# Kernel tuning notes

Hardware: AMD Instinct MI355X
Metric: run time of the kernel (lower is better)

The kernel has to match this reference:

```python
import jax, jax.numpy as jnp
from jax import lax
import numpy as np

B, CIN, CP, H, W = 16, 64, 64, 64, 64
K1 = 3   # deformable kernel
K2 = 5   # parallel conv kernel
EPS = 1e-5


def conv2d(x, w, stride, pad):
    return lax.conv_general_dilated(
        x, w, (stride, stride), [(pad, pad), (pad, pad)],
        dimension_numbers=('NCHW', 'OIHW', 'NCHW'))


def batchnorm(x, g, b, m, v):
    scale = g / jnp.sqrt(v + EPS)
    return (x - m[None, :, None, None]) * scale[None, :, None, None] + b[None, :, None, None]


def deform_conv2d(x, offset, weight, stride, pad):
    # x: [B,Cin,H,W], offset: [B,2*K*K,Ho,Wo] (dy,dx interleaved per kernel tap, torchvision layout)
    Bn, Cin, Hn, Wn = x.shape
    Cout, _, K, _ = weight.shape
    KK = K * K
    Ho, Wo = offset.shape[2], offset.shape[3]
    off = offset.reshape(Bn, KK, 2, Ho, Wo)
    dy, dx = off[:, :, 0], off[:, :, 1]                      # [B,KK,Ho,Wo]
    ky, kx = jnp.meshgrid(jnp.arange(K), jnp.arange(K), indexing='ij')
    ky = ky.reshape(KK).astype(x.dtype)
    kx = kx.reshape(KK).astype(x.dtype)
    base_y = (jnp.arange(Ho) * stride - pad).astype(x.dtype)
    base_x = (jnp.arange(Wo) * stride - pad).astype(x.dtype)
    ys = base_y[None, None, :, None] + ky[None, :, None, None] + dy  # [B,KK,Ho,Wo]
    xs = base_x[None, None, None, :] + kx[None, :, None, None] + dx
    y0 = jnp.floor(ys); x0 = jnp.floor(xs)
    wy1 = ys - y0; wx1 = xs - x0
    wy0 = 1.0 - wy1; wx0 = 1.0 - wx1
    flat = x.reshape(Bn, Cin, Hn * Wn)

    def gather(yi, xi):
        valid = ((yi >= 0) & (yi <= Hn - 1) & (xi >= 0) & (xi <= Wn - 1))
        yc = jnp.clip(yi, 0, Hn - 1).astype(jnp.int32)
        xc = jnp.clip(xi, 0, Wn - 1).astype(jnp.int32)
        idx = (yc * Wn + xc).reshape(Bn, -1)                 # [B,KK*Ho*Wo]
        g = jax.vmap(lambda f, i: jnp.take(f, i, axis=1))(flat, idx)
        g = g.reshape(Bn, Cin, KK, Ho, Wo)
        return g * valid.astype(x.dtype)[:, None]

    val = (gather(y0, x0) * (wy0 * wx0)[:, None]
           + gather(y0, x0 + 1) * (wy0 * wx1)[:, None]
           + gather(y0 + 1, x0) * (wy1 * wx0)[:, None]
           + gather(y0 + 1, x0 + 1) * (wy1 * wx1)[:, None])   # [B,Cin,KK,Ho,Wo]
    w_r = weight.reshape(Cout, Cin, KK)
    return jnp.einsum('bcknm,ock->bonm', val, w_r)


def setup_inputs():
    key = jax.random.key(0)
    ks = jax.random.split(key, 18)
    f32 = jnp.float32
    x = jax.random.normal(ks[0], (B, CIN, H, W), f32)
    w_off = jax.random.normal(ks[1], (2 * K1 * K1, CIN, 3, 3), f32) * 0.01
    b_off = jnp.zeros((2 * K1 * K1,), f32)
    w1 = jax.random.normal(ks[2], (CP, CIN, K1, K1), f32) / np.sqrt(CIN * K1 * K1)
    w3 = jax.random.normal(ks[3], (CP, CIN, K2, K2), f32) / np.sqrt(CIN * K2 * K2)
    w2 = jax.random.normal(ks[4], (CP, CP, 3, 3), f32) / np.sqrt(CP * 9)
    def bn(i):
        g = jax.random.uniform(ks[5 + 4 * i], (CP,), f32, 0.5, 1.5)
        b = jax.random.normal(ks[6 + 4 * i], (CP,), f32) * 0.1
        m = jax.random.normal(ks[7 + 4 * i], (CP,), f32) * 0.1
        v = jax.random.uniform(ks[8 + 4 * i], (CP,), f32, 0.5, 1.5)
        return g, b, m, v
    g1, b1, m1, v1 = bn(0)
    g3, b3, m3, v3 = bn(1)
    g2, b2, m2, v2 = bn(2)
    return dict(x=x, w_off=w_off, b_off=b_off, w1=w1, g1=g1, b1=b1, m1=m1, v1=v1,
                w3=w3, g3=g3, b3=b3, m3=m3, v3=v3, w2=w2, g2=g2, b2=b2, m2=m2, v2=v2)


def reference(x, w_off, b_off, w1, g1, b1, m1, v1, w3, g3, b3, m3, v3, w2, g2, b2, m2, v2):
    offset1 = conv2d(x, w_off, 1, 1) + b_off[None, :, None, None]
    out = jax.nn.relu(batchnorm(deform_conv2d(x, offset1, w1, 1, 1), g1, b1, m1, v1))
    out_1 = jax.nn.relu(batchnorm(conv2d(x, w3, 1, 2), g3, b3, m3, v3))
    out = out + out_1
    out = batchnorm(conv2d(out, w2, 1, 1), g2, b2, m2, v2)
    out = out + x  # identity shortcut (stride=1, in_planes==planes)
    return jax.nn.relu(out)
```

## Files before the change

### kernel.cpp

```cpp
#include <hip/hip_runtime.h>
#include <hip/hip_bf16.h>


#define EPSv 1e-5f
#define XP 68

typedef __attribute__((ext_vector_type(8))) short bf16x8;
typedef __attribute__((ext_vector_type(16))) float f32x16;
typedef __attribute__((ext_vector_type(2))) float f32x2;

__device__ inline ushort f2bf(float f) {
  __hip_bfloat16 h = __float2bfloat16(f);
  return *(ushort*)&h;
}
__device__ inline float bitsf(unsigned int u) {
  union { unsigned int i; float f; } c; c.i = u; return c.f;
}

__global__ __launch_bounds__(256) void prep_kernel(
    const float* __restrict__ x, const float* __restrict__ w3,
    const float* __restrict__ w2, const float* __restrict__ w1,
    const float* __restrict__ w_off,
    ushort* __restrict__ xTp, ushort* __restrict__ w3F,
    ushort* __restrict__ w2F, ushort* __restrict__ w1F,
    ushort* __restrict__ wofF) {
  __shared__ float tile[64][65];
  const int blk = blockIdx.x;
  if (blk < 1024) {
    const int y = blk & 63, b = blk >> 6;
    for (int i = threadIdx.x; i < 4096; i += 256) {
      int ci = i >> 6, xx = i & 63;
      tile[ci][xx] = x[(((size_t)b * 64 + ci) * 64 + y) * 64 + xx];
    }
    __syncthreads();
    for (int i = threadIdx.x; i < 2048; i += 256) {
      int xx = i >> 5, cip = (i & 31) * 2;
      ushort2 v;
      v.x = f2bf(tile[cip][xx]);
      v.y = f2bf(tile[cip + 1][xx]);
      *(ushort2*)&xTp[(((size_t)(b * 64 + y) * XP) + (xx + 2)) * 64 + cip] = v;
    }
    if (threadIdx.x < 128) {
      int colid = threadIdx.x >> 5;
      int col = (colid & 1) + (colid >> 1) * 66;
      int cip = (threadIdx.x & 31) * 2;
      ushort2 z; z.x = 0; z.y = 0;
      *(ushort2*)&xTp[(((size_t)(b * 64 + y) * XP) + col) * 64 + cip] = z;
    }
    return;
  }
  int idx = (blk - 1024) * 256 + threadIdx.x;
  if (idx < 102400) {
    int j = idx & 7, lane = (idx >> 3) & 63, ks = (idx >> 9) & 3;
    int half = (idx >> 11) & 1, kk = idx >> 12;
    int ln = lane & 31, kh = lane >> 5;
    int co = half * 32 + ln, ci = ks * 16 + kh * 8 + j;
    w3F[idx] = f2bf(w3[(co * 64 + ci) * 25 + kk]);
    return;
  }
  idx -= 102400;
  if (idx < 36864) {
    int j = idx & 7, lane = (idx >> 3) & 63, ks = (idx >> 9) & 3;
    int half = (idx >> 11) & 1, kk = idx >> 12;
    int ln = lane & 31, kh = lane >> 5;
    int co = half * 32 + ln, ci = ks * 16 + kh * 8 + j;
    w2F[idx] = f2bf(w2[(co * 64 + ci) * 9 + kk]);
    return;
  }
  idx -= 36864;
  if (idx < 36864) {
    int j = idx & 7, lane = (idx >> 3) & 63, ks = (idx >> 9) & 3;
    int half = (idx >> 11) & 1, kk = idx >> 12;
    int ln = lane & 31, kh = lane >> 5;
    int co = half * 32 + ln, ci = ks * 16 + kh * 8 + j;
    w1F[idx] = f2bf(w1[(co * 64 + ci) * 9 + kk]);
    return;
  }
  idx -= 36864;
  if (idx < 18432) {
    int j = idx & 7, lane = (idx >> 3) & 63, ks = (idx >> 9) & 3;
    int kk = idx >> 11;
    int ln = lane & 31, kh = lane >> 5;
    int ci = ks * 16 + kh * 8 + j;
    wofF[idx] = f2bf(ln < 18 ? w_off[(ln * 64 + ci) * 9 + kk] : 0.f);
  }
}

__device__ __forceinline__ bf16x8 blend4(bf16x8 va, bf16x8 vb, bf16x8 vc, bf16x8 vd,
                                         f32x2 w00v, f32x2 w01v, f32x2 w10v, f32x2 w11v) {
  const unsigned int* ua = (const unsigned int*)&va;
  const unsigned int* ub = (const unsigned int*)&vb;
  const unsigned int* uc = (const unsigned int*)&vc;
  const unsigned int* ud = (const unsigned int*)&vd;
  bf16x8 f;
  ushort2* fo = (ushort2*)&f;
#pragma unroll
  for (int d = 0; d < 4; ++d) {
    f32x2 av = {bitsf(ua[d] << 16), bitsf(ua[d] & 0xFFFF0000u)};
    f32x2 bv = {bitsf(ub[d] << 16), bitsf(ub[d] & 0xFFFF0000u)};
    f32x2 cv = {bitsf(uc[d] << 16), bitsf(uc[d] & 0xFFFF0000u)};
    f32x2 dv = {bitsf(ud[d] << 16), bitsf(ud[d] & 0xFFFF0000u)};
    f32x2 r = w00v * av + w01v * bv + w10v * cv + w11v * dv;
    __hip_bfloat162 h2 = __float22bfloat162_rn(make_float2(r.x, r.y));
    fo[d] = *(ushort2*)&h2;
  }
  return f;
}

__global__ __launch_bounds__(256, 2) void fused_kernel(
    const ushort* __restrict__ xTp, const ushort* __restrict__ wofF,
    const float* __restrict__ b_off, const ushort* __restrict__ w1F,
    const ushort* __restrict__ w3F,
    const float* __restrict__ g1, const float* __restrict__ b1,
    const float* __restrict__ m1, const float* __restrict__ v1,
    const float* __restrict__ g3, const float* __restrict__ b3,
    const float* __restrict__ m3, const float* __restrict__ v3,
    ushort* __restrict__ s1T) {
  __shared__ __align__(16) uint4 ldsx[6 * 68 * 8];
  __shared__ float stash[2 * 64 * 18];
  __shared__ float bn1s[64], bn1b[64], bn3s[64], bn3b[64];

  const int tid = threadIdx.x;
  const int wv = tid >> 6, lane = tid & 63;
  const int ln = lane & 31, kh = lane >> 5;
  const int r = wv >> 1, nt = wv & 1;
  const int y0 = blockIdx.x * 2, b = blockIdx.y;
  const int y = y0 + r, px = nt * 32 + ln;
  const uint4* xT4 = (const uint4*)xTp;
  const ushort* xb = xTp + (size_t)b * 64 * XP * 64;
  const bool interior = (y0 >= 2 && y0 <= 60);

  if (tid < 64) {
    float s = g1[tid] * rsqrtf(v1[tid] + EPSv);
    bn1s[tid] = s; bn1b[tid] = b1[tid] - m1[tid] * s;
    float s3 = g3[tid] * rsqrtf(v3[tid] + EPSv);
    bn3s[tid] = s3; bn3b[tid] = b3[tid] - m3[tid] * s3;
  }
  for (int i = tid; i < 6 * 68 * 8; i += 256) {
    int tr = i / (68 * 8), rem = i % (68 * 8);
    int col = rem >> 3, c = rem & 7;
    int ysrc = min(max(y0 - 2 + tr, 0), 63);
    uint4 v = xT4[((size_t)((b * 64 + ysrc) * XP + col)) * 8 + c];
    ldsx[(tr * 68 + col) * 8 + (c ^ (col & 7))] = v;
  }
  __syncthreads();

  f32x16 acco;
#pragma unroll
  for (int j = 0; j < 16; ++j) acco[j] = 0.f;
  if (interior) {
#pragma unroll
    for (int kk = 0; kk < 9; ++kk) {
      const int ky = kk / 3, kx = kk % 3;
      const int tr = r + ky + 1;
      const int col = px + kx + 1;
      bf16x8 af[4], bf[4];
#pragma unroll
      for (int ks = 0; ks < 4; ++ks)
        af[ks] = *(const bf16x8*)&wofF[(size_t)((kk * 4 + ks) * 64 + lane) * 8];
#pragma unroll
      for (int ks = 0; ks < 4; ++ks) {
        int c = ks * 2 + kh;
        bf[ks] = *(const bf16x8*)&ldsx[(tr * 68 + col) * 8 + (c ^ (col & 7))];
      }
#pragma unroll
      for (int ks = 0; ks < 4; ++ks)
        acco = __builtin_amdgcn_mfma_f32_32x32x16_bf16(af[ks], bf[ks], acco, 0, 0, 0);
    }
  } else {
#pragma unroll
    for (int kk = 0; kk < 9; ++kk) {
      const int ky = kk / 3, kx = kk % 3;
      const int yy = y - 1 + ky;
      if (yy >= 0 && yy <= 63) {
        const int tr = yy - (y0 - 2);
        const int col = px + kx + 1;
#pragma unroll
        for (int ks = 0; ks < 4; ++ks) {
          int c = ks * 2 + kh;
          bf16x8 af = *(const bf16x8*)&wofF[(size_t)((kk * 4 + ks) * 64 + lane) * 8];
          bf16x8 bf = *(const bf16x8*)&ldsx[(tr * 68 + col) * 8 + (c ^ (col & 7))];
          acco = __builtin_amdgcn_mfma_f32_32x32x16_bf16(af, bf, acco, 0, 0, 0);
        }
      }
    }
  }
#pragma unroll
  for (int reg = 0; reg < 16; ++reg) {
    int co = (reg & 3) + 8 * (reg >> 2) + 4 * kh;
    if (co < 18)
      stash[(r * 64 + px) * 18 + co] = acco[reg] + b_off[co];
  }
  asm volatile("" ::: "memory");

  float dyv[9], dxv[9];
#pragma unroll
  for (int kk = 0; kk < 9; ++kk) {
    dyv[kk] = stash[(r * 64 + px) * 18 + 2 * kk];
    dxv[kk] = stash[(r * 64 + px) * 18 + 2 * kk + 1];
  }
  bool fast = true;
#pragma unroll
  for (int kk = 0; kk < 9; ++kk) {
    int iy0 = (int)floorf((float)(y - 1 + kk / 3) + dyv[kk]);
    int iy1 = iy0 + 1;
    bool ok0 = (iy0 < 0) || (iy0 > 63) || (iy0 >= y0 - 2 && iy0 <= y0 + 3);
    bool ok1 = (iy1 < 0) || (iy1 > 63) || (iy1 >= y0 - 2 && iy1 <= y0 + 3);
    fast = fast && ok0 && ok1;
  }

  f32x16 accd0, accd1;
#pragma unroll
  for (int j = 0; j < 16; ++j) { accd0[j] = 0.f; accd1[j] = 0.f; }

  if (__ballot(!fast) == 0ull) {
#pragma unroll
    for (int kk = 0; kk < 9; ++kk) {
      const int ky = kk / 3, kx = kk % 3;
      float ys = (float)(y - 1 + ky) + dyv[kk];
      float xs = (float)(px - 1 + kx) + dxv[kk];
      float y0f = floorf(ys), x0f = floorf(xs);
      float wy1 = ys - y0f, wx1 = xs - x0f;
      float wy0 = 1.f - wy1, wx0 = 1.f - wx1;
      int iy0 = (int)y0f, ix0 = (int)x0f;
      int iy1 = iy0 + 1, ix1 = ix0 + 1;
      float vy0 = (iy0 >= 0 && iy0 <= 63) ? 1.f : 0.f;
      float vy1 = (iy1 >= 0 && iy1 <= 63) ? 1.f : 0.f;
      float vx0 = (ix0 >= 0 && ix0 <= 63) ? 1.f : 0.f;
      float vx1 = (ix1 >= 0 && ix1 <= 63) ? 1.f : 0.f;
      int x0c = min(max(ix0, 0), 63), x1c = min(max(ix1, 0), 63);
      float w00 = wy0 * wx0 * vy0 * vx0;
      float w01 = wy0 * wx1 * vy0 * vx1;
      float w10 = wy1 * wx0 * vy1 * vx0;
      float w11 = wy1 * wx1 * vy1 * vx1;
      int tr0 = min(max(iy0 - (y0 - 2), 0), 5);
      int tr1 = min(max(iy1 - (y0 - 2), 0), 5);
      int c0 = x0c + 2, c1 = x1c + 2;
      f32x2 w00v = {w00, w00}, w01v = {w01, w01};
      f32x2 w10v = {w10, w10}, w11v = {w11, w11};

      bf16x8 a0[4], a1[4], va[4], vb[4], vc[4], vd[4];
#pragma unroll
      for (int ks = 0; ks < 4; ++ks) {
        a0[ks] = *(const bf16x8*)&w1F[(size_t)(((kk * 2 + 0) * 4 + ks) * 64 + lane) * 8];
        a1[ks] = *(const bf16x8*)&w1F[(size_t)(((kk * 2 + 1) * 4 + ks) * 64 + lane) * 8];
      }
#pragma unroll
      for (int ks = 0; ks < 4; ++ks) {
        int c = ks * 2 + kh;
        va[ks] = *(const bf16x8*)&ldsx[(tr0 * 68 + c0) * 8 + (c ^ (c0 & 7))];
        vb[ks] = *(const bf16x8*)&ldsx[(tr0 * 68 + c1) * 8 + (c ^ (c1 & 7))];
        vc[ks] = *(const bf16x8*)&ldsx[(tr1 * 68 + c0) * 8 + (c ^ (c0 & 7))];
        vd[ks] = *(const bf16x8*)&ldsx[(tr1 * 68 + c1) * 8 + (c ^ (c1 & 7))];
      }
#pragma unroll
      for (int ks = 0; ks < 4; ++ks) {
        bf16x8 f = blend4(va[ks], vb[ks], vc[ks], vd[ks], w00v, w01v, w10v, w11v);
        accd0 = __builtin_amdgcn_mfma_f32_32x32x16_bf16(a0[ks], f, accd0, 0, 0, 0);
        accd1 = __builtin_amdgcn_mfma_f32_32x32x16_bf16(a1[ks], f, accd1, 0, 0, 0);
      }
    }
  } else {
#pragma unroll
    for (int kk = 0; kk < 9; ++kk) {
      const int ky = kk / 3, kx = kk % 3;
      float ys = (float)(y - 1 + ky) + dyv[kk];
      float xs = (float)(px - 1 + kx) + dxv[kk];
      float y0f = floorf(ys), x0f = floorf(xs);
      float wy1 = ys - y0f, wx1 = xs - x0f;
      float wy0 = 1.f - wy1, wx0 = 1.f - wx1;
      int iy0 = (int)y0f, ix0 = (int)x0f;
      int iy1 = iy0 + 1, ix1 = ix0 + 1;
      float vy0 = (iy0 >= 0 && iy0 <= 63) ? 1.f : 0.f;
      float vy1 = (iy1 >= 0 && iy1 <= 63) ? 1.f : 0.f;
      float vx0 = (ix0 >= 0 && ix0 <= 63) ? 1.f : 0.f;
      float vx1 = (ix1 >= 0 && ix1 <= 63) ? 1.f : 0.f;
      int x0c = min(max(ix0, 0), 63), x1c = min(max(ix1, 0), 63);
      int y0c = min(max(iy0, 0), 63), y1c = min(max(iy1, 0), 63);
      float w00 = wy0 * wx0 * vy0 * vx0;
      float w01 = wy0 * wx1 * vy0 * vx1;
      float w10 = wy1 * wx0 * vy1 * vx0;
      float w11 = wy1 * wx1 * vy1 * vx1;
      int tr0 = min(max(iy0 - (y0 - 2), 0), 5);
      int tr1 = min(max(iy1 - (y0 - 2), 0), 5);
      int c0 = x0c + 2, c1 = x1c + 2;
      f32x2 w00v = {w00, w00}, w01v = {w01, w01};
      f32x2 w10v = {w10, w10}, w11v = {w11, w11};

      bf16x8 frag[4];
#pragma unroll
      for (int ks = 0; ks < 4; ++ks) {
        int c = ks * 2 + kh;
        bf16x8 va = *(const bf16x8*)&ldsx[(tr0 * 68 + c0) * 8 + (c ^ (c0 & 7))];
        bf16x8 vb = *(const bf16x8*)&ldsx[(tr0 * 68 + c1) * 8 + (c ^ (c1 & 7))];
        bf16x8 vc = *(const bf16x8*)&ldsx[(tr1 * 68 + c0) * 8 + (c ^ (c0 & 7))];
        bf16x8 vd = *(const bf16x8*)&ldsx[(tr1 * 68 + c1) * 8 + (c ^ (c1 & 7))];
        frag[ks] = blend4(va, vb, vc, vd, w00v, w01v, w10v, w11v);
      }
      if (!fast) {
        const ushort* p00 = xb + ((size_t)(y0c * XP + x0c + 2)) * 64 + kh * 8;
        const ushort* p01 = xb + ((size_t)(y0c * XP + x1c + 2)) * 64 + kh * 8;
        const ushort* p10 = xb + ((size_t)(y1c * XP + x0c + 2)) * 64 + kh * 8;
        const ushort* p11 = xb + ((size_t)(y1c * XP + x1c + 2)) * 64 + kh * 8;
#pragma unroll
        for (int ks = 0; ks < 4; ++ks) {
          bf16x8 va = *(const bf16x8*)(p00 + ks * 16);
          bf16x8 vb = *(const bf16x8*)(p01 + ks * 16);
          bf16x8 vc = *(const bf16x8*)(p10 + ks * 16);
          bf16x8 vd = *(const bf16x8*)(p11 + ks * 16);
          frag[ks] = blend4(va, vb, vc, vd, w00v, w01v, w10v, w11v);
        }
      }
#pragma unroll
      for (int ks = 0; ks < 4; ++ks) {
        bf16x8 a0 = *(const bf16x8*)&w1F[(size_t)(((kk * 2 + 0) * 4 + ks) * 64 + lane) * 8];
        bf16x8 a1 = *(const bf16x8*)&w1F[(size_t)(((kk * 2 + 1) * 4 + ks) * 64 + lane) * 8];
        accd0 = __builtin_amdgcn_mfma_f32_32x32x16_bf16(a0, frag[ks], accd0, 0, 0, 0);
        accd1 = __builtin_amdgcn_mfma_f32_32x32x16_bf16(a1, frag[ks], accd1, 0, 0, 0);
      }
    }
  }

  f32x16 acc50, acc51;
#pragma unroll
  for (int j = 0; j < 16; ++j) { acc50[j] = 0.f; acc51[j] = 0.f; }
  if (interior) {
#pragma unroll
    for (int kk = 0; kk < 25; ++kk) {
      const int ky = kk / 5, kx = kk % 5;
      const int tr = r + ky;
      const int col = px + kx;
      bf16x8 a0[4], a1[4], bfv[4];
#pragma unroll
      for (int ks = 0; ks < 4; ++ks) {
        a0[ks] = *(const bf16x8*)&w3F[(size_t)(((kk * 2 + 0) * 4 + ks) * 64 + lane) * 8];
        a1[ks] = *(const bf16x8*)&w3F[(size_t)(((kk * 2 + 1) * 4 + ks) * 64 + lane) * 8];
      }
#pragma unroll
      for (int ks = 0; ks < 4; ++ks) {
        int c = ks * 2 + kh;
        bfv[ks] = *(const bf16x8*)&ldsx[(tr * 68 + col) * 8 + (c ^ (col & 7))];
      }
#pragma unroll
      for (int ks = 0; ks < 4; ++ks) {
        acc50 = __builtin_amdgcn_mfma_f32_32x32x16_bf16(a0[ks], bfv[ks], acc50, 0, 0, 0);
        acc51 = __builtin_amdgcn_mfma_f32_32x32x16_bf16(a1[ks], bfv[ks], acc51, 0, 0, 0);
      }
    }
  } else {
#pragma unroll
    for (int kk = 0; kk < 25; ++kk) {
      const int ky = kk / 5, kx = kk % 5;
      const int yy = y - 2 + ky;
      if (yy >= 0 && yy <= 63) {
        const int tr = r + ky;
        const int col = px + kx;
#pragma unroll
        for (int ks = 0; ks < 4; ++ks) {
          int c = ks * 2 + kh;
          bf16x8 bf = *(const bf16x8*)&ldsx[(tr * 68 + col) * 8 + (c ^ (col & 7))];
          bf16x8 a0 = *(const bf16x8*)&w3F[(size_t)(((kk * 2 + 0) * 4 + ks) * 64 + lane) * 8];
          bf16x8 a1 = *(const bf16x8*)&w3F[(size_t)(((kk * 2 + 1) * 4 + ks) * 64 + lane) * 8];
          acc50 = __builtin_amdgcn_mfma_f32_32x32x16_bf16(a0, bf, acc50, 0, 0, 0);
          acc51 = __builtin_amdgcn_mfma_f32_32x32x16_bf16(a1, bf, acc51, 0, 0, 0);
        }
      }
    }
  }

  ushort* op = s1T + ((size_t)((b * 64 + y) * 64 + px)) * 64;
#pragma unroll
  for (int q = 0; q < 4; ++q) {
    int co0 = 8 * q + 4 * kh;
    float vv[4];
#pragma unroll
    for (int rr = 0; rr < 4; ++rr) {
      int co = co0 + rr;
      float vd = accd0[q * 4 + rr] * bn1s[co] + bn1b[co];
      vd = vd > 0.f ? vd : 0.f;
      float v5 = acc50[q * 4 + rr] * bn3s[co] + bn3b[co];
      v5 = v5 > 0.f ? v5 : 0.f;
      vv[rr] = vd + v5;
    }
    ushort4 st;
    st.x = f2bf(vv[0]); st.y = f2bf(vv[1]); st.z = f2bf(vv[2]); st.w = f2bf(vv[3]);
    *(ushort4*)(op + co0) = st;
#pragma unroll
    for (int rr = 0; rr < 4; ++rr) {
      int co = co0 + 32 + rr;
      float vd = accd1[q * 4 + rr] * bn1s[co] + bn1b[co];
      vd = vd > 0.f ? vd : 0.f;
      float v5 = acc51[q * 4 + rr] * bn3s[co] + bn3b[co];
      v5 = v5 > 0.f ? v5 : 0.f;
      vv[rr] = vd + v5;
    }
    st.x = f2bf(vv[0]); st.y = f2bf(vv[1]); st.z = f2bf(vv[2]); st.w = f2bf(vv[3]);
    *(ushort4*)(op + co0 + 32) = st;
  }
}

__global__ __launch_bounds__(256, 2) void conv3_mfma_kernel(
    const ushort* __restrict__ s1T, const ushort* __restrict__ w2F,
    const float* __restrict__ g2, const float* __restrict__ b2,
    const float* __restrict__ m2, const float* __restrict__ v2,
    const float* __restrict__ x, float* __restrict__ out) {
  __shared__ __align__(16) uint4 Bt[3 * 66 * 8];
  __shared__ float sc[64], bi[64];
  const int tid = threadIdx.x;
  if (tid < 64) {
    float s = g2[tid] * rsqrtf(v2[tid] + EPSv);
    sc[tid] = s;
    bi[tid] = b2[tid] - m2[tid] * s;
  }
  const int y = blockIdx.x, b = blockIdx.y;
  const int wv = tid >> 6, lane = tid & 63;
  const int ln = lane & 31, kh = lane >> 5;
  const int mh = wv & 1, nt = wv >> 1;
  const int px = nt * 32 + ln;
  const uint4* s1T4 = (const uint4*)s1T;

  for (int i = tid; i < 3 * 66 * 8; i += 256) {
    int tr = i / (66 * 8), rem = i % (66 * 8);
    int col = rem >> 3, c = rem & 7;
    int yy = y - 1 + tr, xcol = col - 1;
    uint4 v = make_uint4(0, 0, 0, 0);
    if (yy >= 0 && yy <= 63 && xcol >= 0 && xcol <= 63)
      v = s1T4[((size_t)((b * 64 + yy) * 64 + xcol)) * 8 + c];
    Bt[(tr * 66 + col) * 8 + (c ^ (col & 7))] = v;
  }
  __syncthreads();

  f32x16 acc;
#pragma unroll
  for (int j = 0; j < 16; ++j) acc[j] = 0.f;

#pragma unroll
  for (int kk = 0; kk < 9; ++kk) {
    const int ky = kk / 3, kx = kk % 3;
    const int col = px + kx;
    bf16x8 af[4], bfr[4];
#pragma unroll
    for (int ccb = 0; ccb < 4; ++ccb)
      af[ccb] = *(const bf16x8*)&w2F[(size_t)(((kk * 2 + mh) * 4 + ccb) * 64 + lane) * 8];
#pragma unroll
    for (int ccb = 0; ccb < 4; ++ccb) {
      int c = ccb * 2 + kh;
      bfr[ccb] = *(const bf16x8*)&Bt[(ky * 66 + col) * 8 + (c ^ (col & 7))];
    }
#pragma unroll
    for (int ccb = 0; ccb < 4; ++ccb)
      acc = __builtin_amdgcn_mfma_f32_32x32x16_bf16(af[ccb], bfr[ccb], acc, 0, 0, 0);
  }
#pragma unroll
  for (int reg = 0; reg < 16; ++reg) {
    int co = (reg & 3) + 8 * (reg >> 2) + 4 * kh + mh * 32;
    size_t o = (((size_t)b * 64 + co) * 64 + y) * 64 + px;
    float v = acc[reg] * sc[co] + bi[co] + x[o];
    out[o] = v > 0.f ? v : 0.f;
  }
}

extern "C" void kernel_launch(void* const* d_in, const int* in_sizes, int n_in,
                              void* d_out, int out_size, void* d_ws, size_t ws_size,
                              hipStream_t stream) {
  const float* x     = (const float*)d_in[0];
  const float* w_off = (const float*)d_in[1];
  const float* b_off = (const float*)d_in[2];
  const float* w1    = (const float*)d_in[3];
  const float* g1    = (const float*)d_in[4];
  const float* b1    = (const float*)d_in[5];
  const float* m1    = (const float*)d_in[6];
  const float* v1    = (const float*)d_in[7];
  const float* w3    = (const float*)d_in[8];
  const float* g3    = (const float*)d_in[9];
  const float* b3    = (const float*)d_in[10];
  const float* m3    = (const float*)d_in[11];
  const float* v3    = (const float*)d_in[12];
  const float* w2    = (const float*)d_in[13];
  const float* g2    = (const float*)d_in[14];
  const float* b2    = (const float*)d_in[15];
  const float* m2    = (const float*)d_in[16];
  const float* v2    = (const float*)d_in[17];
  float* out = (float*)d_out;

  ushort* xTp  = (ushort*)d_ws;
  ushort* s1T  = xTp + (size_t)16 * 64 * XP * 64;
  ushort* w3F  = s1T + (size_t)16 * 64 * 64 * 64;
  ushort* w2F  = w3F + 102400;
  ushort* w1F  = w2F + 36864;
  ushort* wofF = w1F + 36864;

  prep_kernel<<<dim3(1024 + 760), dim3(256), 0, stream>>>(x, w3, w2, w1, w_off,
                                                          xTp, w3F, w2F, w1F, wofF);
  fused_kernel<<<dim3(32, 16), dim3(256), 0, stream>>>(xTp, wofF, b_off, w1F, w3F,
                                                       g1, b1, m1, v1, g3, b3, m3, v3,
                                                       s1T);
  conv3_mfma_kernel<<<dim3(64, 16), dim3(256), 0, stream>>>(s1T, w2F, g2, b2, m2, v2,
                                                            x, out);
}
```

Before: 68.02 us.

## Interleave deformable and 5x5 conv MFMA loops; pass offsets via lane shuffles

The offset values produced by the offset conv are now exchanged between the two half-waves with __shfl_xor instead of being staged through an LDS stash array, which removes that shared buffer and its round trip. For interior blocks where all samples fall in the LDS tile, the deformable 3x3 taps and the 5x5 conv taps are interleaved in one loop, so the bilinear blend VALU work can overlap with independent MFMA chains. This keeps four accumulators live at once, which raises register pressure and could hurt occupancy or cause spills.

```diff
diff --git a/kernel.cpp b/kernel.cpp
--- a/kernel.cpp
+++ b/kernel.cpp
@@ -117,7 +117,6 @@
     const float* __restrict__ m3, const float* __restrict__ v3,
     ushort* __restrict__ s1T) {
   __shared__ __align__(16) uint4 ldsx[6 * 68 * 8];
-  __shared__ float stash[2 * 64 * 18];
   __shared__ float bn1s[64], bn1b[64], bn3s[64], bn3b[64];
 
   const int tid = threadIdx.x;
@@ -185,19 +184,20 @@
       }
     }
   }
-#pragma unroll
-  for (int reg = 0; reg < 16; ++reg) {
-    int co = (reg & 3) + 8 * (reg >> 2) + 4 * kh;
-    if (co < 18)
-      stash[(r * 64 + px) * 18 + co] = acco[reg] + b_off[co];
-  }
-  asm volatile("" ::: "memory");
-
+  float oth[10];
+#pragma unroll
+  for (int t = 0; t < 10; ++t) oth[t] = __shfl_xor(acco[t], 32);
   float dyv[9], dxv[9];
 #pragma unroll
   for (int kk = 0; kk < 9; ++kk) {
-    dyv[kk] = stash[(r * 64 + px) * 18 + 2 * kk];
-    dxv[kk] = stash[(r * 64 + px) * 18 + 2 * kk + 1];
+    const int cY = 2 * kk, cX = 2 * kk + 1;
+    const int rY = (cY & 3) + 4 * (cY >> 3);
+    const int rX = (cX & 3) + 4 * (cX >> 3);
+    const int sY = (cY >> 2) & 1, sX = (cX >> 2) & 1;
+    float vy = (sY == kh) ? acco[rY] : oth[rY];
+    float vx = (sX == kh) ? acco[rX] : oth[rX];
+    dyv[kk] = vy + b_off[cY];
+    dxv[kk] = vx + b_off[cX];
   }
   bool fast = true;
 #pragma unroll
@@ -208,161 +208,230 @@
     bool ok1 = (iy1 < 0) || (iy1 > 63) || (iy1 >= y0 - 2 && iy1 <= y0 + 3);
     fast = fast && ok0 && ok1;
   }
-
-  f32x16 accd0, accd1;
-#pragma unroll
-  for (int j = 0; j < 16; ++j) { accd0[j] = 0.f; accd1[j] = 0.f; }
-
-  if (__ballot(!fast) == 0ull) {
-#pragma unroll
-    for (int kk = 0; kk < 9; ++kk) {
-      const int ky = kk / 3, kx = kk % 3;
-      float ys = (float)(y - 1 + ky) + dyv[kk];
-      float xs = (float)(px - 1 + kx) + dxv[kk];
-      float y0f = floorf(ys), x0f = floorf(xs);
-      float wy1 = ys - y0f, wx1 = xs - x0f;
-      float wy0 = 1.f - wy1, wx0 = 1.f - wx1;
-      int iy0 = (int)y0f, ix0 = (int)x0f;
-      int iy1 = iy0 + 1, ix1 = ix0 + 1;
-      float vy0 = (iy0 >= 0 && iy0 <= 63) ? 1.f : 0.f;
-      float vy1 = (iy1 >= 0 && iy1 <= 63) ? 1.f : 0.f;
-      float vx0 = (ix0 >= 0 && ix0 <= 63) ? 1.f : 0.f;
-      float vx1 = (ix1 >= 0 && ix1 <= 63) ? 1.f : 0.f;
-      int x0c = min(max(ix0, 0), 63), x1c = min(max(ix1, 0), 63);
-      float w00 = wy0 * wx0 * vy0 * vx0;
-      float w01 = wy0 * wx1 * vy0 * vx1;
-      float w10 = wy1 * wx0 * vy1 * vx0;
-      float w11 = wy1 * wx1 * vy1 * vx1;
-      int tr0 = min(max(iy0 - (y0 - 2), 0), 5);
-      int tr1 = min(max(iy1 - (y0 - 2), 0), 5);
-      int c0 = x0c + 2, c1 = x1c + 2;
-      f32x2 w00v = {w00, w00}, w01v = {w01, w01};
-      f32x2 w10v = {w10, w10}, w11v = {w11, w11};
-
-      bf16x8 a0[4], a1[4], va[4], vb[4], vc[4], vd[4];
-#pragma unroll
-      for (int ks = 0; ks < 4; ++ks) {
-        a0[ks] = *(const bf16x8*)&w1F[(size_t)(((kk * 2 + 0) * 4 + ks) * 64 + lane) * 8];
-        a1[ks] = *(const bf16x8*)&w1F[(size_t)(((kk * 2 + 1) * 4 + ks) * 64 + lane) * 8];
-      }
-#pragma unroll
-      for (int ks = 0; ks < 4; ++ks) {
-        int c = ks * 2 + kh;
-        va[ks] = *(const bf16x8*)&ldsx[(tr0 * 68 + c0) * 8 + (c ^ (c0 & 7))];
-        vb[ks] = *(const bf16x8*)&ldsx[(tr0 * 68 + c1) * 8 + (c ^ (c1 & 7))];
-        vc[ks] = *(const bf16x8*)&ldsx[(tr1 * 68 + c0) * 8 + (c ^ (c0 & 7))];
-        vd[ks] = *(const bf16x8*)&ldsx[(tr1 * 68 + c1) * 8 + (c ^ (c1 & 7))];
-      }
-#pragma unroll
-      for (int ks = 0; ks < 4; ++ks) {
-        bf16x8 f = blend4(va[ks], vb[ks], vc[ks], vd[ks], w00v, w01v, w10v, w11v);
-        accd0 = __builtin_amdgcn_mfma_f32_32x32x16_bf16(a0[ks], f, accd0, 0, 0, 0);
-        accd1 = __builtin_amdgcn_mfma_f32_32x32x16_bf16(a1[ks], f, accd1, 0, 0, 0);
+  const bool allfast = (__ballot(!fast) == 0ull);
+
+  f32x16 accd0, accd1, acc50, acc51;
+#pragma unroll
+  for (int j = 0; j < 16; ++j) {
+    accd0[j] = 0.f; accd1[j] = 0.f; acc50[j] = 0.f; acc51[j] = 0.f;
+  }
+
+  if (interior && allfast) {
+#pragma unroll
+    for (int dk = 0; dk < 9; ++dk) {
+      {
+        const int ky = dk / 3, kx = dk % 3;
+        float ys = (float)(y - 1 + ky) + dyv[dk];
+        float xs = (float)(px - 1 + kx) + dxv[dk];
+        float y0f = floorf(ys), x0f = floorf(xs);
+        float wy1 = ys - y0f, wx1 = xs - x0f;
+        float wy0 = 1.f - wy1, wx0 = 1.f - wx1;
+        int iy0 = (int)y0f, ix0 = (int)x0f;
+        int iy1 = iy0 + 1, ix1 = ix0 + 1;
+        float vy0 = (iy0 >= 0 && iy0 <= 63) ? 1.f : 0.f;
+        float vy1 = (iy1 >= 0 && iy1 <= 63) ? 1.f : 0.f;
+        float vx0 = (ix0 >= 0 && ix0 <= 63) ? 1.f : 0.f;
+        float vx1 = (ix1 >= 0 && ix1 <= 63) ? 1.f : 0.f;
+        int x0c = min(max(ix0, 0), 63), x1c = min(max(ix1, 0), 63);
+        float w00 = wy0 * wx0 * vy0 * vx0;
+        float w01 = wy0 * wx1 * vy0 * vx1;
+        float w10 = wy1 * wx0 * vy1 * vx0;
+        float w11 = wy1 * wx1 * vy1 * vx1;
+        int tr0 = min(max(iy0 - (y0 - 2), 0), 5);
+        int tr1 = min(max(iy1 - (y0 - 2), 0), 5);
+        int c0 = x0c + 2, c1 = x1c + 2;
+        f32x2 w00v = {w00, w00}, w01v = {w01, w01};
+        f32x2 w10v = {w10, w10}, w11v = {w11, w11};
+
+        bf16x8 a0[4], a1[4], va[4], vb[4], vc[4], vd[4];
+#pragma unroll
+        for (int ks = 0; ks < 4; ++ks) {
+          a0[ks] = *(const bf16x8*)&w1F[(size_t)(((dk * 2 + 0) * 4 + ks) * 64 + lane) * 8];
+          a1[ks] = *(const bf16x8*)&w1F[(size_t)(((dk * 2 + 1) * 4 + ks) * 64 + lane) * 8];
+        }
+#pragma unroll
+        for (int ks = 0; ks < 4; ++ks) {
+          int c = ks * 2 + kh;
+          va[ks] = *(const bf16x8*)&ldsx[(tr0 * 68 + c0) * 8 + (c ^ (c0 & 7))];
+          vb[ks] = *(const bf16x8*)&ldsx[(tr0 * 68 + c1) * 8 + (c ^ (c1 & 7))];
+          vc[ks] = *(const bf16x8*)&ldsx[(tr1 * 68 + c0) * 8 + (c ^ (c0 & 7))];
+          vd[ks] = *(const bf16x8*)&ldsx[(tr1 * 68 + c1) * 8 + (c ^ (c1 & 7))];
+        }
+#pragma unroll
+        for (int ks = 0; ks < 4; ++ks) {
+          bf16x8 f = blend4(va[ks], vb[ks], vc[ks], vd[ks], w00v, w01v, w10v, w11v);
+          accd0 = __builtin_amdgcn_mfma_f32_32x32x16_bf16(a0[ks], f, accd0, 0, 0, 0);
+          accd1 = __builtin_amdgcn_mfma_f32_32x32x16_bf16(a1[ks], f, accd1, 0, 0, 0);
+        }
+      }
+      const int n5 = (dk < 7) ? 3 : 2;
+      const int b5 = (dk < 7) ? dk * 3 : 21 + (dk - 7) * 2;
+#pragma unroll
+      for (int t = 0; t < 3; ++t) {
+        if (t < n5) {
+          const int kk = b5 + t;
+          const int ky5 = kk / 5, kx5 = kk % 5;
+          const int tr = r + ky5;
+          const int col = px + kx5;
+          bf16x8 a0[4], a1[4], bfv[4];
+#pragma unroll
+          for (int ks = 0; ks < 4; ++ks) {
+            a0[ks] = *(const bf16x8*)&w3F[(size_t)(((kk * 2 + 0) * 4 + ks) * 64 + lane) * 8];
+            a1[ks] = *(const bf16x8*)&w3F[(size_t)(((kk * 2 + 1) * 4 + ks) * 64 + lane) * 8];
+          }
+#pragma unroll
+          for (int ks = 0; ks < 4; ++ks) {
+            int c = ks * 2 + kh;
+            bfv[ks] = *(const bf16x8*)&ldsx[(tr * 68 + col) * 8 + (c ^ (col & 7))];
+          }
+#pragma unroll
+          for (int ks = 0; ks < 4; ++ks) {
+            acc50 = __builtin_amdgcn_mfma_f32_32x32x16_bf16(a0[ks], bfv[ks], acc50, 0, 0, 0);
+            acc51 = __builtin_amdgcn_mfma_f32_32x32x16_bf16(a1[ks], bfv[ks], acc51, 0, 0, 0);
+          }
+        }
       }
     }
   } else {
-#pragma unroll
-    for (int kk = 0; kk < 9; ++kk) {
-      const int ky = kk / 3, kx = kk % 3;
-      float ys = (float)(y - 1 + ky) + dyv[kk];
-      float xs = (float)(px - 1 + kx) + dxv[kk];
-      float y0f = floorf(ys), x0f = floorf(xs);
-      float wy1 = ys - y0f, wx1 = xs - x0f;
-      float wy0 = 1.f - wy1, wx0 = 1.f - wx1;
-      int iy0 = (int)y0f, ix0 = (int)x0f;
-      int iy1 = iy0 + 1, ix1 = ix0 + 1;
-      float vy0 = (iy0 >= 0 && iy0 <= 63) ? 1.f : 0.f;
-      float vy1 = (iy1 >= 0 && iy1 <= 63) ? 1.f : 0.f;
-      float vx0 = (ix0 >= 0 && ix0 <= 63) ? 1.f : 0.f;
-      float vx1 = (ix1 >= 0 && ix1 <= 63) ? 1.f : 0.f;
-      int x0c = min(max(ix0, 0), 63), x1c = min(max(ix1, 0), 63);
-      int y0c = min(max(iy0, 0), 63), y1c = min(max(iy1, 0), 63);
-      float w00 = wy0 * wx0 * vy0 * vx0;
-      float w01 = wy0 * wx1 * vy0 * vx1;
-      float w10 = wy1 * wx0 * vy1 * vx0;
-      float w11 = wy1 * wx1 * vy1 * vx1;
-      int tr0 = min(max(iy0 - (y0 - 2), 0), 5);
-      int tr1 = min(max(iy1 - (y0 - 2), 0), 5);
-      int c0 = x0c + 2, c1 = x1c + 2;
-      f32x2 w00v = {w00, w00}, w01v = {w01, w01};
-      f32x2 w10v = {w10, w10}, w11v = {w11, w11};
-
-      bf16x8 frag[4];
-#pragma unroll
-      for (int ks = 0; ks < 4; ++ks) {
-        int c = ks * 2 + kh;
-        bf16x8 va = *(const bf16x8*)&ldsx[(tr0 * 68 + c0) * 8 + (c ^ (c0 & 7))];
-        bf16x8 vb = *(const bf16x8*)&ldsx[(tr0 * 68 + c1) * 8 + (c ^ (c1 & 7))];
-        bf16x8 vc = *(const bf16x8*)&ldsx[(tr1 * 68 + c0) * 8 + (c ^ (c0 & 7))];
-        bf16x8 vd = *(const bf16x8*)&ldsx[(tr1 * 68 + c1) * 8 + (c ^ (c1 & 7))];
-        frag[ks] = blend4(va, vb, vc, vd, w00v, w01v, w10v, w11v);
-      }
-      if (!fast) {
-        const ushort* p00 = xb + ((size_t)(y0c * XP + x0c + 2)) * 64 + kh * 8;
-        const ushort* p01 = xb + ((size_t)(y0c * XP + x1c + 2)) * 64 + kh * 8;
-        const ushort* p10 = xb + ((size_t)(y1c * XP + x0c + 2)) * 64 + kh * 8;
-        const ushort* p11 = xb + ((size_t)(y1c * XP + x1c + 2)) * 64 + kh * 8;
-#pragma unroll
-        for (int ks = 0; ks < 4; ++ks) {
-          bf16x8 va = *(const bf16x8*)(p00 + ks * 16);
-          bf16x8 vb = *(const bf16x8*)(p01 + ks * 16);
-          bf16x8 vc = *(const bf16x8*)(p10 + ks * 16);
-          bf16x8 vd = *(const bf16x8*)(p11 + ks * 16);
+    if (allfast) {
+#pragma unroll
+      for (int kk = 0; kk < 9; ++kk) {
+        const int ky = kk / 3, kx = kk % 3;
+        float ys = (float)(y - 1 + ky) + dyv[kk];
+        float xs = (float)(px - 1 + kx) + dxv[kk];
+        float y0f = floorf(ys), x0f = floorf(xs);
+        float wy1 = ys - y0f, wx1 = xs - x0f;
+        float wy0 = 1.f - wy1, wx0 = 1.f - wx1;
+        int iy0 = (int)y0f, ix0 = (int)x0f;
+        int iy1 = iy0 + 1, ix1 = ix0 + 1;
+        float vy0 = (iy0 >= 0 && iy0 <= 63) ? 1.f : 0.f;
+        float vy1 = (iy1 >= 0 && iy1 <= 63) ? 1.f : 0.f;
+        float vx0 = (ix0 >= 0 && ix0 <= 63) ? 1.f : 0.f;
+        float vx1 = (ix1 >= 0 && ix1 <= 63) ? 1.f : 0.f;
+        int x0c = min(max(ix0, 0), 63), x1c = min(max(ix1, 0), 63);
+        float w00 = wy0 * wx0 * vy0 * vx0;
+        float w01 = wy0 * wx1 * vy0 * vx1;
+        float w10 = wy1 * wx0 * vy1 * vx0;
+        float w11 = wy1 * wx1 * vy1 * vx1;
+        int tr0 = min(max(iy0 - (y0 - 2), 0), 5);
+        int tr1 = min(max(iy1 - (y0 - 2), 0), 5);
+        int c0 = x0c + 2, c1 = x1c + 2;
+        f32x2 w00v = {w00, w00}, w01v = {w01, w01};
+        f32x2 w10v = {w10, w10}, w11v = {w11, w11};
+#pragma unroll
+        for (int ks = 0; ks < 4; ++ks) {
+          int c = ks * 2 + kh;
+          bf16x8 va = *(const bf16x8*)&ldsx[(tr0 * 68 + c0) * 8 + (c ^ (c0 & 7))];
+          bf16x8 vb = *(const bf16x8*)&ldsx[(tr0 * 68 + c1) * 8 + (c ^ (c1 & 7))];
+          bf16x8 vc = *(const bf16x8*)&ldsx[(tr1 * 68 + c0) * 8 + (c ^ (c0 & 7))];
+          bf16x8 vd = *(const bf16x8*)&ldsx[(tr1 * 68 + c1) * 8 + (c ^ (c1 & 7))];
+          bf16x8 f = blend4(va, vb, vc, vd, w00v, w01v, w10v, w11v);
+          bf16x8 a0 = *(const bf16x8*)&w1F[(size_t)(((kk * 2 + 0) * 4 + ks) * 64 + lane) * 8];
+          bf16x8 a1 = *(const bf16x8*)&w1F[(size_t)(((kk * 2 + 1) * 4 + ks) * 64 + lane) * 8];
+          accd0 = __builtin_amdgcn_mfma_f32_32x32x16_bf16(a0, f, accd0, 0, 0, 0);
+          accd1 = __builtin_amdgcn_mfma_f32_32x32x16_bf16(a1, f, accd1, 0, 0, 0);
+        }
+      }
+    } else {
+#pragma unroll
+      for (int kk = 0; kk < 9; ++kk) {
+        const int ky = kk / 3, kx = kk % 3;
+        float ys = (float)(y - 1 + ky) + dyv[kk];
+        float xs = (float)(px - 1 + kx) + dxv[kk];
+        float y0f = floorf(ys), x0f = floorf(xs);
+        float wy1 = ys - y0f, wx1 = xs - x0f;
+        float wy0 = 1.f - wy1, wx0 = 1.f - wx1;
+        int iy0 = (int)y0f, ix0 = (int)x0f;
+        int iy1 = iy0 + 1, ix1 = ix0 + 1;
+        float vy0 = (iy0 >= 0 && iy0 <= 63) ? 1.f : 0.f;
+        float vy1 = (iy1 >= 0 && iy1 <= 63) ? 1.f : 0.f;
+        float vx0 = (ix0 >= 0 && ix0 <= 63) ? 1.f : 0.f;
+        float vx1 = (ix1 >= 0 && ix1 <= 63) ? 1.f : 0.f;
+        int x0c = min(max(ix0, 0), 63), x1c = min(max(ix1, 0), 63);
+        int y0c = min(max(iy0, 0), 63), y1c = min(max(iy1, 0), 63);
+        float w00 = wy0 * wx0 * vy0 * vx0;
+        float w01 = wy0 * wx1 * vy0 * vx1;
+        float w10 = wy1 * wx0 * vy1 * vx0;
+        float w11 = wy1 * wx1 * vy1 * vx1;
+        int tr0 = min(max(iy0 - (y0 - 2), 0), 5);
+        int tr1 = min(max(iy1 - (y0 - 2), 0), 5);
+        int c0 = x0c + 2, c1 = x1c + 2;
+        f32x2 w00v = {w00, w00}, w01v = {w01, w01};
+        f32x2 w10v = {w10, w10}, w11v = {w11, w11};
+
+        bf16x8 frag[4];
+#pragma unroll
+        for (int ks = 0; ks < 4; ++ks) {
+          int c = ks * 2 + kh;
+          bf16x8 va = *(const bf16x8*)&ldsx[(tr0 * 68 + c0) * 8 + (c ^ (c0 & 7))];
+          bf16x8 vb = *(const bf16x8*)&ldsx[(tr0 * 68 + c1) * 8 + (c ^ (c1 & 7))];
+          bf16x8 vc = *(const bf16x8*)&ldsx[(tr1 * 68 + c0) * 8 + (c ^ (c0 & 7))];
+          bf16x8 vd = *(const bf16x8*)&ldsx[(tr1 * 68 + c1) * 8 + (c ^ (c1 & 7))];
           frag[ks] = blend4(va, vb, vc, vd, w00v, w01v, w10v, w11v);
         }
-      }
-#pragma unroll
-      for (int ks = 0; ks < 4; ++ks) {
-        bf16x8 a0 = *(const bf16x8*)&w1F[(size_t)(((kk * 2 + 0) * 4 + ks) * 64 + lane) * 8];
-        bf16x8 a1 = *(const bf16x8*)&w1F[(size_t)(((kk * 2 + 1) * 4 + ks) * 64 + lane) * 8];
-        accd0 = __builtin_amdgcn_mfma_f32_32x32x16_bf16(a0, frag[ks], accd0, 0, 0, 0);
-        accd1 = __builtin_amdgcn_mfma_f32_32x32x16_bf16(a1, frag[ks], accd1, 0, 0, 0);
-      }
-    }
-  }
-
-  f32x16 acc50, acc51;
-#pragma unroll
-  for (int j = 0; j < 16; ++j) { acc50[j] = 0.f; acc51[j] = 0.f; }
-  if (interior) {
-#pragma unroll
-    for (int kk = 0; kk < 25; ++kk) {
-      const int ky = kk / 5, kx = kk % 5;
-      const int tr = r + ky;
-      const int col = px + kx;
-      bf16x8 a0[4], a1[4], bfv[4];
-#pragma unroll
-      for (int ks = 0; ks < 4; ++ks) {
-        a0[ks] = *(const bf16x8*)&w3F[(size_t)(((kk * 2 + 0) * 4 + ks) * 64 + lane) * 8];
-        a1[ks] = *(const bf16x8*)&w3F[(size_t)(((kk * 2 + 1) * 4 + ks) * 64 + lane) * 8];
-      }
-#pragma unroll
-      for (int ks = 0; ks < 4; ++ks) {
-        int c = ks * 2 + kh;
-        bfv[ks] = *(const bf16x8*)&ldsx[(tr * 68 + col) * 8 + (c ^ (col & 7))];
-      }
-#pragma unroll
-      for (int ks = 0; ks < 4; ++ks) {
-        acc50 = __builtin_amdgcn_mfma_f32_32x32x16_bf16(a0[ks], bfv[ks], acc50, 0, 0, 0);
-        acc51 = __builtin_amdgcn_mfma_f32_32x32x16_bf16(a1[ks], bfv[ks], acc51, 0, 0, 0);
-      }
-    }
-  } else {
-#pragma unroll
-    for (int kk = 0; kk < 25; ++kk) {
-      const int ky = kk / 5, kx = kk % 5;
-      const int yy = y - 2 + ky;
-      if (yy >= 0 && yy <= 63) {
+        if (!fast) {
+          const ushort* p00 = xb + ((size_t)(y0c * XP + x0c + 2)) * 64 + kh * 8;
+          const ushort* p01 = xb + ((size_t)(y0c * XP + x1c + 2)) * 64 + kh * 8;
+          const ushort* p10 = xb + ((size_t)(y1c * XP + x0c + 2)) * 64 + kh * 8;
+          const ushort* p11 = xb + ((size_t)(y1c * XP + x1c + 2)) * 64 + kh * 8;
+#pragma unroll
+          for (int ks = 0; ks < 4; ++ks) {
+            bf16x8 va = *(const bf16x8*)(p00 + ks * 16);
+            bf16x8 vb = *(const bf16x8*)(p01 + ks * 16);
+            bf16x8 vc = *(const bf16x8*)(p10 + ks * 16);
+            bf16x8 vd = *(const bf16x8*)(p11 + ks * 16);
+            frag[ks] = blend4(va, vb, vc, vd, w00v, w01v, w10v, w11v);
+          }
+        }
+#pragma unroll
+        for (int ks = 0; ks < 4; ++ks) {
+          bf16x8 a0 = *(const bf16x8*)&w1F[(size_t)(((kk * 2 + 0) * 4 + ks) * 64 + lane) * 8];
+          bf16x8 a1 = *(const bf16x8*)&w1F[(size_t)(((kk * 2 + 1) * 4 + ks) * 64 + lane) * 8];
+          accd0 = __builtin_amdgcn_mfma_f32_32x32x16_bf16(a0, frag[ks], accd0, 0, 0, 0);
+          accd1 = __builtin_amdgcn_mfma_f32_32x32x16_bf16(a1, frag[ks], accd1, 0, 0, 0);
+        }
+      }
+    }
+    if (interior) {
+#pragma unroll
+      for (int kk = 0; kk < 25; ++kk) {
+        const int ky = kk / 5, kx = kk % 5;
         const int tr = r + ky;
         const int col = px + kx;
+        bf16x8 a0[4], a1[4], bfv[4];
+#pragma unroll
+        for (int ks = 0; ks < 4; ++ks) {
+          a0[ks] = *(const bf16x8*)&w3F[(size_t)(((kk * 2 + 0) * 4 + ks) * 64 + lane) * 8];
+          a1[ks] = *(const bf16x8*)&w3F[(size_t)(((kk * 2 + 1) * 4 + ks) * 64 + lane) * 8];
+        }
 #pragma unroll
         for (int ks = 0; ks < 4; ++ks) {
           int c = ks * 2 + kh;
-          bf16x8 bf = *(const bf16x8*)&ldsx[(tr * 68 + col) * 8 + (c ^ (col & 7))];
-          bf16x8 a0 = *(const bf16x8*)&w3F[(size_t)(((kk * 2 + 0) * 4 + ks) * 64 + lane) * 8];
-          bf16x8 a1 = *(const bf16x8*)&w3F[(size_t)(((kk * 2 + 1) * 4 + ks) * 64 + lane) * 8];
-          acc50 = __builtin_amdgcn_mfma_f32_32x32x16_bf16(a0, bf, acc50, 0, 0, 0);
-          acc51 = __builtin_amdgcn_mfma_f32_32x32x16_bf16(a1, bf, acc51, 0, 0, 0);
+          bfv[ks] = *(const bf16x8*)&ldsx[(tr * 68 + col) * 8 + (c ^ (col & 7))];
+        }
+#pragma unroll
+        for (int ks = 0; ks < 4; ++ks) {
+          acc50 = __builtin_amdgcn_mfma_f32_32x32x16_bf16(a0[ks], bfv[ks], acc50, 0, 0, 0);
+          acc51 = __builtin_amdgcn_mfma_f32_32x32x16_bf16(a1[ks], bfv[ks], acc51, 0, 0, 0);
+        }
+      }
+    } else {
+#pragma unroll
+      for (int kk = 0; kk < 25; ++kk) {
+        const int ky = kk / 5, kx = kk % 5;
+        const int yy = y - 2 + ky;
+        if (yy >= 0 && yy <= 63) {
+          const int tr = r + ky;
+          const int col = px + kx;
+#pragma unroll
+          for (int ks = 0; ks < 4; ++ks) {
+            int c = ks * 2 + kh;
+            bf16x8 bf = *(const bf16x8*)&ldsx[(tr * 68 + col) * 8 + (c ^ (col & 7))];
+            bf16x8 a0 = *(const bf16x8*)&w3F[(size_t)(((kk * 2 + 0) * 4 + ks) * 64 + lane) * 8];
+            bf16x8 a1 = *(const bf16x8*)&w3F[(size_t)(((kk * 2 + 1) * 4 + ks) * 64 + lane) * 8];
+            acc50 = __builtin_amdgcn_mfma_f32_32x32x16_bf16(a0, bf, acc50, 0, 0, 0);
+            acc51 = __builtin_amdgcn_mfma_f32_32x32x16_bf16(a1, bf, acc51, 0, 0, 0);
+          }
         }
       }
     }
```

New measurement: 66.99 us. Within noise of the previous version (-1.5%).
